# Kernel optimization log

Measured on AMD Instinct MI355X. Metric: run time of the kernel, lower is better.

Reference implementation:

```python
import jax, jax.numpy as jnp
import numpy as np

SHAPES = ((100, 100), (50, 50), (25, 25), (13, 13))
LENS = [h * w for h, w in SHAPES]
STARTS = [0]
for n in LENS[:-1]:
    STARTS.append(STARTS[-1] + n)
S_TOT = sum(LENS)  # 13294
B, C, HH, DH, L, P, NQ, NL, FF = 2, 256, 8, 32, 4, 4, 300, 6, 1024
WH = np.array([[w, h] for h, w in SHAPES], np.float32)  # [L,2] (W,H) offset normalizer


def ln(x, g, b):
    m = x.mean(-1, keepdims=True)
    v = ((x - m) ** 2).mean(-1, keepdims=True)
    return (x - m) * jax.lax.rsqrt(v + 1e-5) * g + b


def bilinear(v, grid):
    # v: [N,Hl,Wl,D]; grid: [N,Q,2] in [-1,1]; grid_sample bilinear, align_corners=False, zero padding
    N, Hl, Wl, Dd = v.shape
    x = (grid[..., 0] + 1.0) * 0.5 * Wl - 0.5
    y = (grid[..., 1] + 1.0) * 0.5 * Hl - 0.5
    x0f = jnp.floor(x); y0f = jnp.floor(y)
    wx = x - x0f; wy = y - y0f
    x0 = x0f.astype(jnp.int32); y0 = y0f.astype(jnp.int32)
    vf = v.reshape(N, Hl * Wl, Dd)
    def g(yi, xi):
        valid = (yi >= 0) & (yi < Hl) & (xi >= 0) & (xi < Wl)
        idx = jnp.clip(yi, 0, Hl - 1) * Wl + jnp.clip(xi, 0, Wl - 1)
        return jnp.take_along_axis(vf, idx[..., None], axis=1) * valid[..., None]
    return (((1 - wy) * (1 - wx))[..., None] * g(y0, x0)
            + ((1 - wy) * wx)[..., None] * g(y0, x0 + 1)
            + (wy * (1 - wx))[..., None] * g(y0 + 1, x0)
            + (wy * wx)[..., None] * g(y0 + 1, x0 + 1))


def msda(query, ref, src, so_w, so_b, aw_w, aw_b, vp_w, vp_b, op_w, op_b):
    # query:[B,Lq,C] ref:[B,Lq,L,2] src:[B,S,C]
    Bq, Lq, _ = query.shape
    value = (src @ vp_w.T + vp_b).reshape(Bq, S_TOT, HH, DH)
    offs = (query @ so_w.T + so_b).reshape(Bq, Lq, HH, L, P, 2)
    aw = jax.nn.softmax((query @ aw_w.T + aw_b).reshape(Bq, Lq, HH, L * P), -1)
    aw = aw.reshape(Bq, Lq, HH, L, P)
    loc = ref[:, :, None, :, None, :] + offs / jnp.asarray(WH)[None, None, None, :, None, :]
    grid = 2.0 * loc - 1.0  # [B,Lq,HH,L,P,2]
    out = jnp.zeros((Bq, HH, Lq, DH), query.dtype)
    for l, (Hl, Wl) in enumerate(SHAPES):
        st = STARTS[l]
        v_l = value[:, st:st + Hl * Wl].reshape(Bq, Hl, Wl, HH, DH).transpose(0, 3, 1, 2, 4).reshape(Bq * HH, Hl, Wl, DH)
        g_l = grid[:, :, :, l].transpose(0, 2, 1, 3, 4).reshape(Bq * HH, Lq * P, 2)
        s = bilinear(v_l, g_l).reshape(Bq, HH, Lq, P, DH)
        out = out + jnp.einsum('bqhp,bhqpd->bhqd', aw[:, :, :, l], s)
    out = out.transpose(0, 2, 1, 3).reshape(Bq, Lq, C)
    return out @ op_w.T + op_b


def enc_ref_points():
    refs = []
    for Hl, Wl in SHAPES:
        ry = (jnp.arange(Hl, dtype=jnp.float32) + 0.5) / Hl
        rx = (jnp.arange(Wl, dtype=jnp.float32) + 0.5) / Wl
        gy, gx = jnp.meshgrid(ry, rx, indexing='ij')
        refs.append(jnp.stack([gx.reshape(-1), gy.reshape(-1)], -1))
    r = jnp.concatenate(refs, 0)  # [S,2]; valid_ratios == 1 (no padding)
    return jnp.broadcast_to(r[None, :, None, :], (B, S_TOT, L, 2))


def _forward(src_flatten, pos_flatten, query_embed, level_embed, refp_w, refp_b,
             eso_w, eso_b, eaw_w, eaw_b, evp_w, evp_b, eop_w, eop_b,
             en1_g, en1_b, el1_w, el1_b, el2_w, el2_b, en2_g, en2_b,
             dso_w, dso_b, daw_w, daw_b, dvp_w, dvp_b, dop_w, dop_b,
             dsa_in_w, dsa_in_b, dsa_out_w, dsa_out_b,
             dn1_g, dn1_b, dn2_g, dn2_b, dn3_g, dn3_b,
             dl1_w, dl1_b, dl2_w, dl2_b):
    lev = jnp.concatenate([jnp.broadcast_to(level_embed[l], (LENS[l], C)) for l in range(L)], 0)
    pos = pos_flatten + lev[None]
    memory = src_flatten
    eref = enc_ref_points()
    for i in range(NL):  # encoder
        q = memory + pos
        m2 = msda(q, eref, memory, eso_w[i], eso_b[i], eaw_w[i], eaw_b[i], evp_w[i], evp_b[i], eop_w[i], eop_b[i])
        memory = ln(memory + m2, en1_g[i], en1_b[i])
        f = jax.nn.relu(memory @ el1_w[i].T + el1_b[i]) @ el2_w[i].T + el2_b[i]
        memory = ln(memory + f, en2_g[i], en2_b[i])
    qpos, tgt = jnp.split(query_embed, 2, axis=-1)
    qpos = jnp.broadcast_to(qpos[None], (B, NQ, C))
    tgt = jnp.broadcast_to(tgt[None], (B, NQ, C))
    ref = jax.nn.sigmoid(qpos @ refp_w.T + refp_b)  # [B,NQ,2]
    init_ref = ref
    ref_in = jnp.broadcast_to(ref[:, :, None, :], (B, NQ, L, 2))
    scale = 1.0 / np.sqrt(DH)
    for i in range(NL):  # decoder
        q = tgt + qpos
        wq, wk, wv = jnp.split(dsa_in_w[i], 3, 0)
        bq, bk, bv = jnp.split(dsa_in_b[i], 3, 0)
        qh = (q @ wq.T + bq).reshape(B, NQ, HH, DH).transpose(0, 2, 1, 3)
        kh = (q @ wk.T + bk).reshape(B, NQ, HH, DH).transpose(0, 2, 1, 3)
        vh = (tgt @ wv.T + bv).reshape(B, NQ, HH, DH).transpose(0, 2, 1, 3)
        att = jax.nn.softmax(jnp.einsum('bhqd,bhkd->bhqk', qh, kh) * scale, -1)
        sa = jnp.einsum('bhqk,bhkd->bhqd', att, vh).transpose(0, 2, 1, 3).reshape(B, NQ, C)
        sa = sa @ dsa_out_w[i].T + dsa_out_b[i]
        tgt = ln(tgt + sa, dn2_g[i], dn2_b[i])
        ca = msda(tgt + qpos, ref_in, memory, dso_w[i], dso_b[i], daw_w[i], daw_b[i], dvp_w[i], dvp_b[i], dop_w[i], dop_b[i])
        tgt = ln(tgt + ca, dn1_g[i], dn1_b[i])
        f = jax.nn.relu(tgt @ dl1_w[i].T + dl1_b[i]) @ dl2_w[i].T + dl2_b[i]
        tgt = ln(tgt + f, dn3_g[i], dn3_b[i])
    return tgt, init_ref, ref


def setup_inputs() -> dict:
    ks = iter(jax.random.split(jax.random.key(0), 80))
    def rn(shape, s=0.02):
        return jax.random.normal(next(ks), shape, jnp.float32) * s
    z = lambda shape: jnp.zeros(shape, jnp.float32)
    o = lambda shape: jnp.ones(shape, jnp.float32)
    HLP2, HLP = HH * L * P * 2, HH * L * P
    return {
        'src_flatten': rn((B, S_TOT, C), 1.0),
        'pos_flatten': rn((B, S_TOT, C), 1.0),
        'query_embed': rn((NQ, 2 * C), 1.0),
        'level_embed': rn((L, C), 1.0),
        'refp_w': rn((2, C)), 'refp_b': z((2,)),
        'eso_w': rn((NL, HLP2, C)), 'eso_b': z((NL, HLP2)),
        'eaw_w': rn((NL, HLP, C)), 'eaw_b': z((NL, HLP)),
        'evp_w': rn((NL, C, C)), 'evp_b': z((NL, C)),
        'eop_w': rn((NL, C, C)), 'eop_b': z((NL, C)),
        'en1_g': o((NL, C)), 'en1_b': z((NL, C)),
        'el1_w': rn((NL, FF, C)), 'el1_b': z((NL, FF)),
        'el2_w': rn((NL, C, FF)), 'el2_b': z((NL, C)),
        'en2_g': o((NL, C)), 'en2_b': z((NL, C)),
        'dso_w': rn((NL, HLP2, C)), 'dso_b': z((NL, HLP2)),
        'daw_w': rn((NL, HLP, C)), 'daw_b': z((NL, HLP)),
        'dvp_w': rn((NL, C, C)), 'dvp_b': z((NL, C)),
        'dop_w': rn((NL, C, C)), 'dop_b': z((NL, C)),
        'dsa_in_w': rn((NL, 3 * C, C)), 'dsa_in_b': z((NL, 3 * C)),
        'dsa_out_w': rn((NL, C, C)), 'dsa_out_b': z((NL, C)),
        'dn1_g': o((NL, C)), 'dn1_b': z((NL, C)),
        'dn2_g': o((NL, C)), 'dn2_b': z((NL, C)),
        'dn3_g': o((NL, C)), 'dn3_b': z((NL, C)),
        'dl1_w': rn((NL, FF, C)), 'dl1_b': z((NL, FF)),
        'dl2_w': rn((NL, C, FF)), 'dl2_b': z((NL, C)),
    }


def reference(src_flatten, pos_flatten, query_embed, level_embed, refp_w, refp_b,
              eso_w, eso_b, eaw_w, eaw_b, evp_w, evp_b, eop_w, eop_b,
              en1_g, en1_b, el1_w, el1_b, el2_w, el2_b, en2_g, en2_b,
              dso_w, dso_b, daw_w, daw_b, dvp_w, dvp_b, dop_w, dop_b,
              dsa_in_w, dsa_in_b, dsa_out_w, dsa_out_b,
              dn1_g, dn1_b, dn2_g, dn2_b, dn3_g, dn3_b,
              dl1_w, dl1_b, dl2_w, dl2_b):
    return _forward(src_flatten, pos_flatten, query_embed, level_embed, refp_w, refp_b,
                    eso_w, eso_b, eaw_w, eaw_b, evp_w, evp_b, eop_w, eop_b,
                    en1_g, en1_b, el1_w, el1_b, el2_w, el2_b, en2_g, en2_b,
                    dso_w, dso_b, daw_w, daw_b, dvp_w, dvp_b, dop_w, dop_b,
                    dsa_in_w, dsa_in_b, dsa_out_w, dsa_out_b,
                    dn1_g, dn1_b, dn2_g, dn2_b, dn3_g, dn3_b,
                    dl1_w, dl1_b, dl2_w, dl2_b)
```

## Files before the change

### kernel.cpp

```cpp
#include <hip/hip_runtime.h>

static constexpr int kS  = 13294;
static constexpr int kB  = 2;
static constexpr int kBS = kB * kS;
static constexpr int kC  = 256;
static constexpr int kH  = 8;
static constexpr int kNQ = 300;
static constexpr int kFF = 1024;
static constexpr int kNL = 6;

using short8 = __attribute__((ext_vector_type(8))) short;
using f32x4  = __attribute__((ext_vector_type(4))) float;

__device__ __forceinline__ unsigned short f2b(float f) {
  unsigned u = __builtin_bit_cast(unsigned, f);
  return (unsigned short)((u + 0x7FFF + ((u >> 16) & 1)) >> 16);
}
__device__ __forceinline__ float bf2f(unsigned short u) {
  return __builtin_bit_cast(float, ((unsigned)u) << 16);
}
__device__ __forceinline__ float bflo(unsigned u) {
  return __builtin_bit_cast(float, u << 16);
}
__device__ __forceinline__ float bfhi(unsigned u) {
  return __builtin_bit_cast(float, u & 0xFFFF0000u);
}

#if defined(__has_builtin)
#if __has_builtin(__builtin_amdgcn_global_load_lds)
#define HAS_GLL 1
#endif
#endif
#ifndef HAS_GLL
#define HAS_GLL 0
#endif

#if HAS_GLL
typedef const __attribute__((address_space(1))) void* gas_t;
typedef __attribute__((address_space(3))) void* las_t;
#define GLOAD16(gp, lp) __builtin_amdgcn_global_load_lds((gas_t)(gp), (las_t)(lp), 16, 0, 0)
#endif

template<int ACT, int OBF>
__global__ __launch_bounds__(256) void gemm_mfma(
    const unsigned short* __restrict__ A, const unsigned short* __restrict__ Wt,
    const float* __restrict__ bias, void* __restrict__ outp, int M, int N, int K) {
  __shared__ __align__(16) unsigned short As[128 * 64];
  __shared__ __align__(16) unsigned short Bs[128 * 64];
  const int t = threadIdx.x;
  const int nB = N >> 7;
  const int tot = gridDim.x;
  const int q8 = tot >> 3, r8 = tot & 7;
  const int xcd = blockIdx.x & 7, pos = blockIdx.x >> 3;
  const int wg = (xcd < r8 ? xcd * (q8 + 1) : r8 * (q8 + 1) + (xcd - r8) * q8) + pos;
  const int m0 = (wg / nB) * 128, n0 = (wg % nB) * 128;
  const int wid = t >> 6, lane = t & 63;
  const int wr = wid >> 1, wc = wid & 1;
  const int srow = t >> 3;
  const int scol = (t & 7) * 8;
  const int lr = lane & 15;
  const int lk = (lane >> 4) * 8;

  f32x4 acc[4][4];
#pragma unroll
  for (int i = 0; i < 4; ++i)
#pragma unroll
    for (int j = 0; j < 4; ++j) acc[i][j] = (f32x4){0.f, 0.f, 0.f, 0.f};

  for (int k0 = 0; k0 < K; k0 += 64) {
#if HAS_GLL
    __syncthreads();
#pragma unroll
    for (int c = 0; c < 4; ++c) {
      int ar = m0 + c * 32 + srow; if (ar >= M) ar = M - 1;
      GLOAD16(A + (size_t)ar * K + k0 + scol, (char*)As + c * 4096 + t * 16);
      int br = n0 + c * 32 + srow; if (br >= N) br = N - 1;
      GLOAD16(Wt + (size_t)br * K + k0 + scol, (char*)Bs + c * 4096 + t * 16);
    }
    __syncthreads();
#else
    short8 ta[4], tb[4];
#pragma unroll
    for (int c = 0; c < 4; ++c) {
      int ar = m0 + c * 32 + srow; if (ar >= M) ar = M - 1;
      ta[c] = *(const short8*)(A + (size_t)ar * K + k0 + scol);
      int br = n0 + c * 32 + srow; if (br >= N) br = N - 1;
      tb[c] = *(const short8*)(Wt + (size_t)br * K + k0 + scol);
    }
    __syncthreads();
#pragma unroll
    for (int c = 0; c < 4; ++c) {
      *(short8*)&As[c * 2048 + t * 8] = ta[c];
      *(short8*)&Bs[c * 2048 + t * 8] = tb[c];
    }
    __syncthreads();
#endif
#pragma unroll
    for (int kk = 0; kk < 2; ++kk) {
      short8 af[4], bf[4];
#pragma unroll
      for (int mi = 0; mi < 4; ++mi)
        af[mi] = *(const short8*)&As[(wr * 64 + mi * 16 + lr) * 64 + kk * 32 + lk];
#pragma unroll
      for (int ni = 0; ni < 4; ++ni)
        bf[ni] = *(const short8*)&Bs[(wc * 64 + ni * 16 + lr) * 64 + kk * 32 + lk];
#pragma unroll
      for (int mi = 0; mi < 4; ++mi)
#pragma unroll
        for (int ni = 0; ni < 4; ++ni)
          acc[mi][ni] = __builtin_amdgcn_mfma_f32_16x16x32_bf16(af[mi], bf[ni], acc[mi][ni], 0, 0, 0);
    }
  }
  const int orow0 = m0 + wr * 64;
  const int ocol = n0 + wc * 64 + (lane & 15);
  float bv[4];
#pragma unroll
  for (int ni = 0; ni < 4; ++ni) bv[ni] = bias[ocol + ni * 16];
#pragma unroll
  for (int mi = 0; mi < 4; ++mi) {
#pragma unroll
    for (int j = 0; j < 4; ++j) {
      const int r = orow0 + mi * 16 + (lane >> 4) * 4 + j;
      if (r < M) {
#pragma unroll
        for (int ni = 0; ni < 4; ++ni) {
          float v = acc[mi][ni][j] + bv[ni];
          if (ACT) v = fmaxf(v, 0.f);
          if (OBF) ((unsigned short*)outp)[(size_t)r * N + ocol + ni * 16] = f2b(v);
          else     ((float*)outp)[(size_t)r * N + ocol + ni * 16] = v;
        }
      }
    }
  }
}

template<int ACT, int OBF>
__global__ __launch_bounds__(256) void gemm_mfma_s(
    const unsigned short* __restrict__ A, const unsigned short* __restrict__ Wt,
    const float* __restrict__ bias, void* __restrict__ outp, int M, int N, int K) {
  __shared__ __align__(16) unsigned short As[64 * 64];
  __shared__ __align__(16) unsigned short Bs[64 * 64];
  const int t = threadIdx.x;
  const int m0 = blockIdx.y * 64, n0 = blockIdx.x * 64;
  const int wid = t >> 6, lane = t & 63;
  const int wr = wid >> 1, wc = wid & 1;
  const int srow = t >> 3;
  const int scol = (t & 7) * 8;
  const int lr = lane & 15;
  const int lk = (lane >> 4) * 8;

  f32x4 acc[2][2];
#pragma unroll
  for (int i = 0; i < 2; ++i)
#pragma unroll
    for (int j = 0; j < 2; ++j) acc[i][j] = (f32x4){0.f, 0.f, 0.f, 0.f};

  for (int k0 = 0; k0 < K; k0 += 64) {
#if HAS_GLL
    __syncthreads();
#pragma unroll
    for (int c = 0; c < 2; ++c) {
      int ar = m0 + c * 32 + srow; if (ar >= M) ar = M - 1;
      GLOAD16(A + (size_t)ar * K + k0 + scol, (char*)As + c * 4096 + t * 16);
      int br = n0 + c * 32 + srow; if (br >= N) br = N - 1;
      GLOAD16(Wt + (size_t)br * K + k0 + scol, (char*)Bs + c * 4096 + t * 16);
    }
    __syncthreads();
#else
    short8 ta[2], tb[2];
#pragma unroll
    for (int c = 0; c < 2; ++c) {
      int ar = m0 + c * 32 + srow; if (ar >= M) ar = M - 1;
      ta[c] = *(const short8*)(A + (size_t)ar * K + k0 + scol);
      int br = n0 + c * 32 + srow; if (br >= N) br = N - 1;
      tb[c] = *(const short8*)(Wt + (size_t)br * K + k0 + scol);
    }
    __syncthreads();
#pragma unroll
    for (int c = 0; c < 2; ++c) {
      *(short8*)&As[c * 2048 + t * 8] = ta[c];
      *(short8*)&Bs[c * 2048 + t * 8] = tb[c];
    }
    __syncthreads();
#endif
#pragma unroll
    for (int kk = 0; kk < 2; ++kk) {
      short8 af[2], bf[2];
#pragma unroll
      for (int mi = 0; mi < 2; ++mi)
        af[mi] = *(const short8*)&As[(wr * 32 + mi * 16 + lr) * 64 + kk * 32 + lk];
#pragma unroll
      for (int ni = 0; ni < 2; ++ni)
        bf[ni] = *(const short8*)&Bs[(wc * 32 + ni * 16 + lr) * 64 + kk * 32 + lk];
#pragma unroll
      for (int mi = 0; mi < 2; ++mi)
#pragma unroll
        for (int ni = 0; ni < 2; ++ni)
          acc[mi][ni] = __builtin_amdgcn_mfma_f32_16x16x32_bf16(af[mi], bf[ni], acc[mi][ni], 0, 0, 0);
    }
  }
  const int orow0 = m0 + wr * 32;
  const int ocol = n0 + wc * 32 + (lane & 15);
  float bv[2];
#pragma unroll
  for (int ni = 0; ni < 2; ++ni) bv[ni] = bias[ocol + ni * 16];
#pragma unroll
  for (int mi = 0; mi < 2; ++mi) {
#pragma unroll
    for (int j = 0; j < 4; ++j) {
      const int r = orow0 + mi * 16 + (lane >> 4) * 4 + j;
      if (r < M) {
#pragma unroll
        for (int ni = 0; ni < 2; ++ni) {
          float v = acc[mi][ni][j] + bv[ni];
          if (ACT) v = fmaxf(v, 0.f);
          if (OBF) ((unsigned short*)outp)[(size_t)r * N + ocol + ni * 16] = f2b(v);
          else     ((float*)outp)[(size_t)r * N + ocol + ni * 16] = v;
        }
      }
    }
  }
}

template<int WRITEQ>
__global__ __launch_bounds__(256) void gemm_ln_k(
    const unsigned short* __restrict__ A, const unsigned short* __restrict__ Wt,
    const float* __restrict__ bias, const float* __restrict__ x,
    const float* __restrict__ g, const float* __restrict__ be,
    float* __restrict__ outf, unsigned short* __restrict__ outb,
    unsigned short* __restrict__ qout, const float* __restrict__ pos,
    const float* __restrict__ lev, int M, int K) {
  __shared__ __align__(16) unsigned short As[64 * 64];
  __shared__ __align__(16) unsigned short Bs[256 * 64];
  __shared__ float rsum[64][4], rsq[64][4], rmv[64][2];
  const int t = threadIdx.x;
  const int m0 = blockIdx.x * 64;
  const int wid = t >> 6, lane = t & 63;
  const int srow = t >> 3;
  const int scol = (t & 7) * 8;
  const int lr = lane & 15;
  const int q4 = lane >> 4;
  const int lk = q4 * 8;

  f32x4 acc[4][4];
#pragma unroll
  for (int i = 0; i < 4; ++i)
#pragma unroll
    for (int j = 0; j < 4; ++j) acc[i][j] = (f32x4){0.f, 0.f, 0.f, 0.f};

  for (int k0 = 0; k0 < K; k0 += 64) {
#if HAS_GLL
    __syncthreads();
#pragma unroll
    for (int c = 0; c < 2; ++c) {
      int ar = m0 + c * 32 + srow; if (ar >= M) ar = M - 1;
      GLOAD16(A + (size_t)ar * K + k0 + scol, (char*)As + c * 4096 + t * 16);
    }
#pragma unroll
    for (int c = 0; c < 8; ++c) {
      GLOAD16(Wt + (size_t)(c * 32 + srow) * K + k0 + scol, (char*)Bs + c * 4096 + t * 16);
    }
    __syncthreads();
#else
    short8 ta[2], tb[8];
#pragma unroll
    for (int c = 0; c < 2; ++c) {
      int ar = m0 + c * 32 + srow; if (ar >= M) ar = M - 1;
      ta[c] = *(const short8*)(A + (size_t)ar * K + k0 + scol);
    }
#pragma unroll
    for (int c = 0; c < 8; ++c)
      tb[c] = *(const short8*)(Wt + (size_t)(c * 32 + srow) * K + k0 + scol);
    __syncthreads();
#pragma unroll
    for (int c = 0; c < 2; ++c) *(short8*)&As[c * 2048 + t * 8] = ta[c];
#pragma unroll
    for (int c = 0; c < 8; ++c) *(short8*)&Bs[c * 2048 + t * 8] = tb[c];
    __syncthreads();
#endif
#pragma unroll
    for (int kk = 0; kk < 2; ++kk) {
      short8 af[4], bf[4];
#pragma unroll
      for (int mi = 0; mi < 4; ++mi)
        af[mi] = *(const short8*)&As[(mi * 16 + lr) * 64 + kk * 32 + lk];
#pragma unroll
      for (int ni = 0; ni < 4; ++ni)
        bf[ni] = *(const short8*)&Bs[(wid * 64 + ni * 16 + lr) * 64 + kk * 32 + lk];
#pragma unroll
      for (int mi = 0; mi < 4; ++mi)
#pragma unroll
        for (int ni = 0; ni < 4; ++ni)
          acc[mi][ni] = __builtin_amdgcn_mfma_f32_16x16x32_bf16(af[mi], bf[ni], acc[mi][ni], 0, 0, 0);
    }
  }
  float bv[4], gv[4], bev[4];
  int cols[4];
#pragma unroll
  for (int ni = 0; ni < 4; ++ni) {
    cols[ni] = wid * 64 + ni * 16 + lr;
    bv[ni] = bias[cols[ni]];
    gv[ni] = g[cols[ni]];
    bev[ni] = be[cols[ni]];
  }
#pragma unroll
  for (int mi = 0; mi < 4; ++mi) {
#pragma unroll
    for (int j = 0; j < 4; ++j) {
      const int brow = mi * 16 + q4 * 4 + j;
      int grow = m0 + brow; if (grow >= M) grow = M - 1;
      const float* xr = x + (size_t)grow * 256;
      float s = 0.f, s2 = 0.f;
#pragma unroll
      for (int ni = 0; ni < 4; ++ni) {
        float v = acc[mi][ni][j] + bv[ni] + xr[cols[ni]];
        acc[mi][ni][j] = v;
        s += v; s2 += v * v;
      }
#pragma unroll
      for (int o = 1; o < 16; o <<= 1) {
        s += __shfl_xor(s, o);
        s2 += __shfl_xor(s2, o);
      }
      if (lr == 0) { rsum[brow][wid] = s; rsq[brow][wid] = s2; }
    }
  }
  __syncthreads();
  if (t < 64) {
    float s = rsum[t][0] + rsum[t][1] + rsum[t][2] + rsum[t][3];
    float s2 = rsq[t][0] + rsq[t][1] + rsq[t][2] + rsq[t][3];
    float mean = s * (1.f / 256.f);
    float var = s2 * (1.f / 256.f) - mean * mean;
    rmv[t][0] = mean;
    rmv[t][1] = rsqrtf(var + 1e-5f);
  }
  __syncthreads();
#pragma unroll
  for (int mi = 0; mi < 4; ++mi) {
#pragma unroll
    for (int j = 0; j < 4; ++j) {
      const int brow = mi * 16 + q4 * 4 + j;
      const int grow = m0 + brow;
      if (grow >= M) continue;
      const float mean = rmv[brow][0], rs = rmv[brow][1];
      int levl = 0;
      if (WRITEQ) {
        int srow_g = (grow >= kS) ? grow - kS : grow;
        levl = (srow_g < 10000) ? 0 : (srow_g < 12500) ? 1 : (srow_g < 13125) ? 2 : 3;
      }
#pragma unroll
      for (int ni = 0; ni < 4; ++ni) {
        const float v = (acc[mi][ni][j] - mean) * rs * gv[ni] + bev[ni];
        const size_t oi = (size_t)grow * 256 + cols[ni];
        outf[oi] = v;
        outb[oi] = f2b(v);
        if (WRITEQ) {
          const float qv = v + pos[oi] + lev[levl * 256 + cols[ni]];
          qout[oi] = f2b(qv);
        }
      }
    }
  }
}

__global__ void cast_bf_k(const float* __restrict__ in, unsigned short* __restrict__ out, int n4) {
  int i = blockIdx.x * 256 + threadIdx.x;
  if (i >= n4) return;
  float4 v = ((const float4*)in)[i];
  ushort4 o; o.x = f2b(v.x); o.y = f2b(v.y); o.z = f2b(v.z); o.w = f2b(v.w);
  ((ushort4*)out)[i] = o;
}

__global__ void copy_cast_k(const float* __restrict__ in, float* __restrict__ outf,
                            unsigned short* __restrict__ outb, int n4) {
  int i = blockIdx.x * 256 + threadIdx.x;
  if (i >= n4) return;
  float4 v = ((const float4*)in)[i];
  ((float4*)outf)[i] = v;
  ushort4 o; o.x = f2b(v.x); o.y = f2b(v.y); o.z = f2b(v.z); o.w = f2b(v.w);
  ((ushort4*)outb)[i] = o;
}

__global__ void pack_bias_k(const float* __restrict__ so_b, const float* __restrict__ aw_b,
                            float* __restrict__ fb) {
  int i = blockIdx.x * 256 + threadIdx.x;
  if (i >= kNL * 384) return;
  int l = i / 384, j = i - l * 384;
  fb[i] = (j < 256) ? so_b[l * 256 + j] : aw_b[l * 128 + j - 256];
}

__global__ void enc_q_k(const float* __restrict__ mem, const float* __restrict__ pos,
                        const float* __restrict__ lev, unsigned short* __restrict__ q, int n4) {
  int i = blockIdx.x * 256 + threadIdx.x;
  if (i >= n4) return;
  int c4 = i & 63;
  int row = i >> 6;
  int s = row % kS;
  int l = (s < 10000) ? 0 : (s < 12500) ? 1 : (s < 13125) ? 2 : 3;
  float4 m = ((const float4*)mem)[i];
  float4 p = ((const float4*)pos)[i];
  float4 lv = ((const float4*)(lev + l * kC))[c4];
  ushort4 o;
  o.x = f2b(m.x + p.x + lv.x); o.y = f2b(m.y + p.y + lv.y);
  o.z = f2b(m.z + p.z + lv.z); o.w = f2b(m.w + p.w + lv.w);
  ((ushort4*)q)[i] = o;
}

__global__ void refs_k(float* __restrict__ refS) {
  int s = blockIdx.x * 256 + threadIdx.x;
  if (s >= kS) return;
  int st, W;
  if (s < 10000)      { st = 0;     W = 100; }
  else if (s < 12500) { st = 10000; W = 50; }
  else if (s < 13125) { st = 12500; W = 25; }
  else                { st = 13125; W = 13; }
  int idx = s - st;
  int y = idx / W;
  int x = idx - y * W;
  refS[s * 2 + 0] = (x + 0.5f) / (float)W;
  refS[s * 2 + 1] = (y + 0.5f) / (float)W;
}

__global__ __launch_bounds__(256) void msda_fused_k(
    const unsigned short* __restrict__ value, int vstride, int vcol,
    const unsigned short* __restrict__ foab, const float* __restrict__ refs,
    unsigned short* __restrict__ out, int Mq) {
  __shared__ int   sidx[16][2][kH][4];
  __shared__ float sw[16][2][kH][4];
  const int t = threadIdx.x;
  const int bq0 = blockIdx.x * 2;
  const int qq = t >> 7;
  {
    const int bq = bq0 + qq;
    const int b = (bq >= Mq) ? 1 : 0;
    const int qi = bq - b * Mq;
    const int h = (t >> 4) & 7, lp = t & 15, l = lp >> 2;
    const unsigned short* row = foab + (size_t)bq * 384;
    float logit = bf2f(row[256 + h * 16 + lp]);
    float mx = logit;
#pragma unroll
    for (int o = 1; o < 16; o <<= 1) mx = fmaxf(mx, __shfl_xor(mx, o));
    float e = __expf(logit - mx), ssum = e;
#pragma unroll
    for (int o = 1; o < 16; o <<= 1) ssum += __shfl_xor(ssum, o);
    const float a = e / ssum;
    const unsigned opair = *(const unsigned*)(row + h * 32 + lp * 2);
    const float offx = bflo(opair);
    const float offy = bfhi(opair);
    const float rx = refs[qi * 2 + 0];
    const float ry = refs[qi * 2 + 1];
    const int wtab[4] = {100, 50, 25, 13};
    const int stab[4] = {0, 10000, 12500, 13125};
    const int W = wtab[l];
    const int start = stab[l];
    const float px = fmaf(rx, (float)W, offx) - 0.5f;
    const float py = fmaf(ry, (float)W, offy) - 0.5f;
    const float fx = floorf(px), fy = floorf(py);
    const float wx = px - fx, wy = py - fy;
    const int x0 = (int)fx, y0 = (int)fy;
    const int x0c = min(max(x0, 0), W - 1);
    const int x1c = min(max(x0 + 1, 0), W - 1);
    const int y0c = min(max(y0, 0), W - 1);
    const int y1c = min(max(y0 + 1, 0), W - 1);
    const float vx0 = (x0 >= 0 && x0 < W) ? 1.f : 0.f;
    const float vx1 = (x0 + 1 >= 0 && x0 + 1 < W) ? 1.f : 0.f;
    const float vy0 = (y0 >= 0 && y0 < W) ? 1.f : 0.f;
    const float vy1 = (y0 + 1 >= 0 && y0 + 1 < W) ? 1.f : 0.f;
    const int base0 = b * kS * vstride + vcol + start * vstride;
    sidx[lp][qq][h][0] = base0 + (y0c * W + x0c) * vstride;
    sidx[lp][qq][h][1] = base0 + (y0c * W + x1c) * vstride;
    sidx[lp][qq][h][2] = base0 + (y1c * W + x0c) * vstride;
    sidx[lp][qq][h][3] = base0 + (y1c * W + x1c) * vstride;
    const float omwx = 1.f - wx, omwy = 1.f - wy;
    sw[lp][qq][h][0] = a * omwy * omwx * vy0 * vx0;
    sw[lp][qq][h][1] = a * omwy * wx * vy0 * vx1;
    sw[lp][qq][h][2] = a * wy * omwx * vy1 * vx0;
    sw[lp][qq][h][3] = a * wy * wx * vy1 * vx1;
  }
  __syncthreads();
  const int h = (t >> 4) & 7, dp = t & 15;
  const int bq = bq0 + qq;
  const int chan = h * 64 + dp * 4;
  const char* valc = (const char*)value;
  float aLo0 = 0.f, aLo1 = 0.f, aHi0 = 0.f, aHi1 = 0.f;
#pragma unroll
  for (int p0 = 0; p0 < 16; p0 += 8) {
    unsigned u[32];
    float w[32];
#pragma unroll
    for (int pp = 0; pp < 8; ++pp) {
      const int4 I = *(const int4*)&sidx[p0 + pp][qq][h][0];
      const float4 Wv = *(const float4*)&sw[p0 + pp][qq][h][0];
      u[pp * 4 + 0] = *(const unsigned*)(valc + (unsigned)(I.x + chan));
      u[pp * 4 + 1] = *(const unsigned*)(valc + (unsigned)(I.y + chan));
      u[pp * 4 + 2] = *(const unsigned*)(valc + (unsigned)(I.z + chan));
      u[pp * 4 + 3] = *(const unsigned*)(valc + (unsigned)(I.w + chan));
      w[pp * 4 + 0] = Wv.x; w[pp * 4 + 1] = Wv.y;
      w[pp * 4 + 2] = Wv.z; w[pp * 4 + 3] = Wv.w;
    }
#pragma unroll
    for (int j = 0; j < 32; j += 2) {
      aLo0 = fmaf(w[j], bflo(u[j]), aLo0);
      aHi0 = fmaf(w[j], bfhi(u[j]), aHi0);
      aLo1 = fmaf(w[j + 1], bflo(u[j + 1]), aLo1);
      aHi1 = fmaf(w[j + 1], bfhi(u[j + 1]), aHi1);
    }
  }
  const float accLo = aLo0 + aLo1;
  const float accHi = aHi0 + aHi1;
  const unsigned packed = (unsigned)f2b(accLo) | ((unsigned)f2b(accHi) << 16);
  ((unsigned*)out)[(size_t)bq * 128 + h * 16 + dp] = packed;
}

__global__ void add_bcast_bf_k(const float* __restrict__ a, const float* __restrict__ b,
                               unsigned short* __restrict__ out, int n4, int nb4) {
  int i = blockIdx.x * 256 + threadIdx.x;
  if (i >= n4) return;
  const float4 av = ((const float4*)a)[i];
  const float4 bv = ((const float4*)b)[i % nb4];
  ushort4 o;
  o.x = f2b(av.x + bv.x); o.y = f2b(av.y + bv.y);
  o.z = f2b(av.z + bv.z); o.w = f2b(av.w + bv.w);
  ((ushort4*)out)[i] = o;
}

__global__ void dec_init_k(const float* __restrict__ qe, float* __restrict__ tgt,
                           unsigned short* __restrict__ tgt_bf, float* __restrict__ qposb) {
  int i = blockIdx.x * 256 + threadIdx.x;
  if (i >= kNQ * kC) return;
  int q = i >> 8, c = i & 255;
  qposb[i] = qe[q * 512 + c];
  float tg = qe[q * 512 + 256 + c];
  tgt[i] = tg;
  tgt[kNQ * kC + i] = tg;
  unsigned short tb = f2b(tg);
  tgt_bf[i] = tb;
  tgt_bf[kNQ * kC + i] = tb;
}

__global__ __launch_bounds__(64) void ref_k(const float* __restrict__ qposb,
                                            const float* __restrict__ rw,
                                            const float* __restrict__ rb,
                                            float* __restrict__ ref300) {
  const int q = blockIdx.x;
  const int lane = threadIdx.x;
  const float4 qv = ((const float4*)(qposb + q * 256))[lane];
  const float4 w0 = ((const float4*)rw)[lane];
  const float4 w1 = ((const float4*)(rw + 256))[lane];
  float a0 = qv.x * w0.x + qv.y * w0.y + qv.z * w0.z + qv.w * w0.w;
  float a1 = qv.x * w1.x + qv.y * w1.y + qv.z * w1.z + qv.w * w1.w;
#pragma unroll
  for (int off = 32; off; off >>= 1) {
    a0 += __shfl_xor(a0, off);
    a1 += __shfl_xor(a1, off);
  }
  if (lane == 0) {
    ref300[q * 2 + 0] = 1.f / (1.f + __expf(-(a0 + rb[0])));
    ref300[q * 2 + 1] = 1.f / (1.f + __expf(-(a1 + rb[1])));
  }
}

__global__ __launch_bounds__(64) void dec_attn_k(const float* __restrict__ qk,
                                                 const float* __restrict__ v,
                                                 unsigned short* __restrict__ outp) {
  const int bid = blockIdx.x;
  const int q = bid % kNQ;
  const int bh = bid / kNQ;
  const int h = bh & 7;
  const int b = bh >> 3;
  const int lane = threadIdx.x;
  __shared__ float p[304];
  const float* qv = qk + ((size_t)(b * kNQ + q)) * 512 + h * 32;
  float qreg[32];
#pragma unroll
  for (int m = 0; m < 32; ++m) qreg[m] = qv[m];
  float scores[5];
  float mx = -1e30f;
#pragma unroll
  for (int j = 0; j < 5; ++j) {
    const int k = lane + j * 64;
    float sc = -1e30f;
    if (k < kNQ) {
      const float* kv = qk + ((size_t)(b * kNQ + k)) * 512 + 256 + h * 32;
      float acc = 0.f;
#pragma unroll
      for (int m = 0; m < 32; ++m) acc = fmaf(qreg[m], kv[m], acc);
      sc = acc * 0.17677669529663687f;
    }
    scores[j] = sc;
    mx = fmaxf(mx, sc);
  }
#pragma unroll
  for (int off = 32; off; off >>= 1) mx = fmaxf(mx, __shfl_xor(mx, off));
  float sum = 0.f;
#pragma unroll
  for (int j = 0; j < 5; ++j) {
    const int k = lane + j * 64;
    float e = 0.f;
    if (k < kNQ) e = __expf(scores[j] - mx);
    scores[j] = e;
    sum += e;
  }
#pragma unroll
  for (int off = 32; off; off >>= 1) sum += __shfl_xor(sum, off);
  const float inv = 1.f / sum;
#pragma unroll
  for (int j = 0; j < 5; ++j) {
    const int k = lane + j * 64;
    if (k < kNQ) p[k] = scores[j] * inv;
  }
  __syncthreads();
  const int d = lane & 31, half = lane >> 5;
  float acc = 0.f;
  for (int k = half * 150; k < half * 150 + 150; ++k)
    acc = fmaf(p[k], v[((size_t)(b * kNQ + k)) * 256 + h * 32 + d], acc);
  acc += __shfl_down(acc, 32);
  if (lane < 32) outp[((size_t)(b * kNQ + q)) * 256 + h * 32 + d] = f2b(acc);
}

__global__ void write_refs_k(const float* __restrict__ ref300, float* __restrict__ outp) {
  int i = blockIdx.x * 256 + threadIdx.x;
  if (i >= 1200) return;
  float v = ref300[i % 600];
  outp[153600 + i] = v;
  outp[154800 + i] = v;
}

__global__ void sentinel_k(float* __restrict__ outp) {
  if (threadIdx.x < 64) outp[threadIdx.x] = 12345.0f;
}

extern "C" void kernel_launch(void* const* d_in, const int* in_sizes, int n_in,
                              void* d_out, int out_size, void* d_ws, size_t ws_size,
                              hipStream_t stream) {
  const float* src      = (const float*)d_in[0];
  const float* pos      = (const float*)d_in[1];
  const float* qe       = (const float*)d_in[2];
  const float* lev      = (const float*)d_in[3];
  const float* refp_w   = (const float*)d_in[4];
  const float* refp_b   = (const float*)d_in[5];
  const float* eso_w    = (const float*)d_in[6];
  const float* eso_b    = (const float*)d_in[7];
  const float* eaw_w    = (const float*)d_in[8];
  const float* eaw_b    = (const float*)d_in[9];
  const float* evp_w    = (const float*)d_in[10];
  const float* evp_b    = (const float*)d_in[11];
  const float* eop_w    = (const float*)d_in[12];
  const float* eop_b    = (const float*)d_in[13];
  const float* en1_g    = (const float*)d_in[14];
  const float* en1_b    = (const float*)d_in[15];
  const float* el1_w    = (const float*)d_in[16];
  const float* el1_b    = (const float*)d_in[17];
  const float* el2_w    = (const float*)d_in[18];
  const float* el2_b    = (const float*)d_in[19];
  const float* en2_g    = (const float*)d_in[20];
  const float* en2_b    = (const float*)d_in[21];
  const float* dso_w    = (const float*)d_in[22];
  const float* dso_b    = (const float*)d_in[23];
  const float* daw_w    = (const float*)d_in[24];
  const float* daw_b    = (const float*)d_in[25];
  const float* dvp_w    = (const float*)d_in[26];
  const float* dvp_b    = (const float*)d_in[27];
  const float* dop_w    = (const float*)d_in[28];
  const float* dop_b    = (const float*)d_in[29];
  const float* dsa_in_w = (const float*)d_in[30];
  const float* dsa_in_b = (const float*)d_in[31];
  const float* dsa_out_w= (const float*)d_in[32];
  const float* dsa_out_b= (const float*)d_in[33];
  const float* dn1_g    = (const float*)d_in[34];
  const float* dn1_b    = (const float*)d_in[35];
  const float* dn2_g    = (const float*)d_in[36];
  const float* dn2_b    = (const float*)d_in[37];
  const float* dn3_g    = (const float*)d_in[38];
  const float* dn3_b    = (const float*)d_in[39];
  const float* dl1_w    = (const float*)d_in[40];
  const float* dl1_b    = (const float*)d_in[41];
  const float* dl2_w    = (const float*)d_in[42];
  const float* dl2_b    = (const float*)d_in[43];

  float* Wsp = (float*)d_ws;
  size_t off = 0;
  auto alloc = [&](size_t n) { float* p = Wsp + off; off += n; return p; };
  const size_t NBC = (size_t)kBS * kC;
  float* memory   = alloc(NBC);
  unsigned short* memory_bf = (unsigned short*)alloc(NBC / 2);
  float* r2       = alloc(NBC);
  unsigned short* val_bf = (unsigned short*)r2;
  float* r3       = alloc(NBC / 2);
  unsigned short* qbuf_bf = (unsigned short*)r3;
  unsigned short* sampbuf_bf = (unsigned short*)r3;
  float* r4       = alloc(NBC * 2);
  unsigned short* foab_bf = (unsigned short*)r4;
  unsigned short* hid_bf = (unsigned short*)r4;
  unsigned short* val_all = (unsigned short*)r2;
  float* refS     = alloc((size_t)kS * 2 + 2);
  auto allocb = [&](size_t elems) { return (unsigned short*)alloc(elems / 2); };
  unsigned short* fesoawW = allocb((size_t)kNL * 384 * 256);
  unsigned short* evpW  = allocb((size_t)kNL * 65536);
  unsigned short* eopW  = allocb((size_t)kNL * 65536);
  unsigned short* el1W  = allocb((size_t)kNL * 262144);
  unsigned short* el2W  = allocb((size_t)kNL * 262144);
  unsigned short* fdsoawW = allocb((size_t)kNL * 384 * 256);
  unsigned short* dvpW  = allocb((size_t)kNL * 65536);
  unsigned short* dopW  = allocb((size_t)kNL * 65536);
  unsigned short* dsaiW = allocb((size_t)kNL * 196608);
  unsigned short* dsaoW = allocb((size_t)kNL * 65536);
  unsigned short* dl1W  = allocb((size_t)kNL * 262144);
  unsigned short* dl2W  = allocb((size_t)kNL * 262144);
  float* fbias_e  = alloc((size_t)kNL * 384);
  float* fbias_d  = alloc((size_t)kNL * 384);
  const size_t NQC = (size_t)kB * kNQ * kC;
  float* tgt      = alloc(NQC);
  unsigned short* tgt_bf = (unsigned short*)alloc(NQC / 2);
  float* qposb    = alloc((size_t)kNQ * kC);
  unsigned short* dq_bf = (unsigned short*)alloc(NQC / 2);
  float* qkbuf    = alloc(NQC * 2);
  float* vbuf     = alloc(NQC);
  unsigned short* sabuf_bf = (unsigned short*)alloc(NQC / 2);
  unsigned short* dfoab_bf = (unsigned short*)alloc((size_t)kB * kNQ * 384 / 2);
  unsigned short* dsamp_bf = (unsigned short*)alloc(NQC / 2);
  unsigned short* dffnh_bf = (unsigned short*)alloc((size_t)kB * kNQ * kFF / 2);
  float* ref300   = alloc(600);

  if (ws_size < off * sizeof(float)) {
    hipLaunchKernelGGL(sentinel_k, dim3(1), dim3(64), 0, stream, (float*)d_out);
    return;
  }

  auto GEMM = [&](const unsigned short* A, const unsigned short* Wt, const float* bias,
                  void* out, int M, int N, int K, int variant) {
    dim3 g((N / 128) * ((M + 127) / 128));
    if (variant == 1)
      hipLaunchKernelGGL((gemm_mfma<1, 1>), g, dim3(256), 0, stream, A, Wt, bias, out, M, N, K);
    else if (variant == 2)
      hipLaunchKernelGGL((gemm_mfma<0, 1>), g, dim3(256), 0, stream, A, Wt, bias, out, M, N, K);
    else
      hipLaunchKernelGGL((gemm_mfma<0, 0>), g, dim3(256), 0, stream, A, Wt, bias, out, M, N, K);
  };
  auto GEMMS = [&](const unsigned short* A, const unsigned short* Wt, const float* bias,
                   void* out, int M, int N, int K, int variant) {
    dim3 g(N / 64, (M + 63) / 64);
    if (variant == 1)
      hipLaunchKernelGGL((gemm_mfma_s<1, 1>), g, dim3(256), 0, stream, A, Wt, bias, out, M, N, K);
    else if (variant == 2)
      hipLaunchKernelGGL((gemm_mfma_s<0, 1>), g, dim3(256), 0, stream, A, Wt, bias, out, M, N, K);
    else
      hipLaunchKernelGGL((gemm_mfma_s<0, 0>), g, dim3(256), 0, stream, A, Wt, bias, out, M, N, K);
  };
  auto CASTW = [&](const float* srcw, unsigned short* dstw, size_t elems) {
    int n4 = (int)(elems / 4);
    hipLaunchKernelGGL(cast_bf_k, dim3((n4 + 255) / 256), dim3(256), 0, stream, srcw, dstw, n4);
  };

  for (int i = 0; i < kNL; ++i) {
    CASTW(eso_w + (size_t)i * 65536, fesoawW + (size_t)i * 98304, 65536);
    CASTW(eaw_w + (size_t)i * 32768, fesoawW + (size_t)i * 98304 + 65536, 32768);
    CASTW(dso_w + (size_t)i * 65536, fdsoawW + (size_t)i * 98304, 65536);
    CASTW(daw_w + (size_t)i * 32768, fdsoawW + (size_t)i * 98304 + 65536, 32768);
  }
  CASTW(evp_w, evpW, (size_t)kNL * 65536);
  CASTW(eop_w, eopW, (size_t)kNL * 65536);
  CASTW(el1_w, el1W, (size_t)kNL * 262144);
  CASTW(el2_w, el2W, (size_t)kNL * 262144);
  CASTW(dvp_w, dvpW, (size_t)kNL * 65536);
  CASTW(dop_w, dopW, (size_t)kNL * 65536);
  CASTW(dsa_in_w, dsaiW, (size_t)kNL * 196608);
  CASTW(dsa_out_w, dsaoW, (size_t)kNL * 65536);
  CASTW(dl1_w, dl1W, (size_t)kNL * 262144);
  CASTW(dl2_w, dl2W, (size_t)kNL * 262144);
  hipLaunchKernelGGL(pack_bias_k, dim3((kNL * 384 + 255) / 256), dim3(256), 0, stream,
                     eso_b, eaw_b, fbias_e);
  hipLaunchKernelGGL(pack_bias_k, dim3((kNL * 384 + 255) / 256), dim3(256), 0, stream,
                     dso_b, daw_b, fbias_d);
  const int n4full = kBS * 64;
  hipLaunchKernelGGL(copy_cast_k, dim3((n4full + 255) / 256), dim3(256), 0, stream,
                     src, memory, memory_bf, n4full);
  hipLaunchKernelGGL(refs_k, dim3((kS + 255) / 256), dim3(256), 0, stream, refS);
  hipLaunchKernelGGL(enc_q_k, dim3((n4full + 255) / 256), dim3(256), 0, stream,
                     memory, pos, lev, qbuf_bf, n4full);

  const int grid_ln = (kBS + 63) / 64;
  for (int i = 0; i < kNL; ++i) {
    GEMM(memory_bf, evpW + (size_t)i * 65536, evp_b + i * kC, val_bf, kBS, 256, 256, 2);
    GEMM(qbuf_bf, fesoawW + (size_t)i * 98304, fbias_e + i * 384, foab_bf, kBS, 384, 256, 2);
    hipLaunchKernelGGL(msda_fused_k, dim3(kBS / 2), dim3(256), 0, stream,
                       val_bf, 512, 0, foab_bf, refS, sampbuf_bf, kS);
    hipLaunchKernelGGL((gemm_ln_k<0>), dim3(grid_ln), dim3(256), 0, stream,
                       sampbuf_bf, eopW + (size_t)i * 65536, eop_b + i * kC,
                       memory, en1_g + i * kC, en1_b + i * kC,
                       memory, memory_bf, (unsigned short*)nullptr,
                       (const float*)nullptr, (const float*)nullptr, kBS, 256);
    GEMM(memory_bf, el1W + (size_t)i * 262144, el1_b + i * kFF, hid_bf, kBS, 1024, 256, 1);
    hipLaunchKernelGGL((gemm_ln_k<1>), dim3(grid_ln), dim3(256), 0, stream,
                       hid_bf, el2W + (size_t)i * 262144, el2_b + i * kC,
                       memory, en2_g + i * kC, en2_b + i * kC,
                       memory, memory_bf, qbuf_bf, pos, lev, kBS, 1024);
  }

  hipLaunchKernelGGL(dec_init_k, dim3(300), dim3(256), 0, stream, qe, tgt, tgt_bf, qposb);
  hipLaunchKernelGGL(ref_k, dim3(kNQ), dim3(64), 0, stream, qposb, refp_w, refp_b, ref300);
  GEMM(memory_bf, dvpW, dvp_b, val_all, kBS, kNL * 256, 256, 2);

  const int dn4 = kB * kNQ * 64;
  const int qn4 = kNQ * 64;
  const int MD = kB * kNQ;
  const int grid_lnd = (MD + 63) / 64;
  for (int i = 0; i < kNL; ++i) {
    hipLaunchKernelGGL(add_bcast_bf_k, dim3((dn4 + 255) / 256), dim3(256), 0, stream,
                       tgt, qposb, dq_bf, dn4, qn4);
    GEMMS(dq_bf, dsaiW + (size_t)i * 196608, dsa_in_b + i * 768, qkbuf, MD, 512, 256, 0);
    GEMMS(tgt_bf, dsaiW + (size_t)i * 196608 + (size_t)512 * 256,
          dsa_in_b + i * 768 + 512, vbuf, MD, 256, 256, 0);
    hipLaunchKernelGGL(dec_attn_k, dim3(kB * kH * kNQ), dim3(64), 0, stream,
                       qkbuf, vbuf, sabuf_bf);
    hipLaunchKernelGGL((gemm_ln_k<0>), dim3(grid_lnd), dim3(256), 0, stream,
                       sabuf_bf, dsaoW + (size_t)i * 65536, dsa_out_b + i * kC,
                       tgt, dn2_g + i * kC, dn2_b + i * kC,
                       tgt, tgt_bf, (unsigned short*)nullptr,
                       (const float*)nullptr, (const float*)nullptr, MD, 256);
    hipLaunchKernelGGL(add_bcast_bf_k, dim3((dn4 + 255) / 256), dim3(256), 0, stream,
                       tgt, qposb, dq_bf, dn4, qn4);
    GEMMS(dq_bf, fdsoawW + (size_t)i * 98304, fbias_d + i * 384, dfoab_bf, MD, 384, 256, 2);
    hipLaunchKernelGGL(msda_fused_k, dim3(MD / 2), dim3(256), 0, stream,
                       val_all, kNL * 512, i * 512, dfoab_bf, ref300, dsamp_bf, kNQ);
    hipLaunchKernelGGL((gemm_ln_k<0>), dim3(grid_lnd), dim3(256), 0, stream,
                       dsamp_bf, dopW + (size_t)i * 65536, dop_b + i * kC,
                       tgt, dn1_g + i * kC, dn1_b + i * kC,
                       tgt, tgt_bf, (unsigned short*)nullptr,
                       (const float*)nullptr, (const float*)nullptr, MD, 256);
    GEMMS(tgt_bf, dl1W + (size_t)i * 262144, dl1_b + i * kFF, dffnh_bf, MD, 1024, 256, 1);
    hipLaunchKernelGGL((gemm_ln_k<0>), dim3(grid_lnd), dim3(256), 0, stream,
                       dffnh_bf, dl2W + (size_t)i * 262144, dl2_b + i * kC,
                       tgt, dn3_g + i * kC, dn3_b + i * kC,
                       tgt, tgt_bf, (unsigned short*)nullptr,
                       (const float*)nullptr, (const float*)nullptr, MD, 1024);
  }

  hipMemcpyAsync(d_out, tgt, NQC * sizeof(float), hipMemcpyDeviceToDevice, stream);
  hipLaunchKernelGGL(write_refs_k, dim3(5), dim3(256), 0, stream, ref300, (float*)d_out);
}
```

Measured before the change: 2.051 ms.

## Keep encoder residual stream in bf16 only and halve GEMM-LN row tile

Drops the fp32 encoder memory buffer: the fused GEMM+LayerNorm now reads the residual input as bf16 and writes only bf16 output unless WRITEF is set. Precomputes pos+level embedding once as a bf16 buffer instead of recomputing level index and reading two fp32 arrays every layer. Also shrinks the GEMM-LN tile from 64 to 32 rows so more blocks launch. This cuts memory traffic per encoder layer but loses precision in the residual stream, since the residual is rounded to bf16 every layer, and the decoder's residual input is also read from bf16.

```diff
diff --git a/kernel.cpp b/kernel.cpp
--- a/kernel.cpp
+++ b/kernel.cpp
@@ -222,19 +222,19 @@
   }
 }
 
-template<int WRITEQ>
+template<int WRITEQ, int WRITEF>
 __global__ __launch_bounds__(256) void gemm_ln_k(
     const unsigned short* __restrict__ A, const unsigned short* __restrict__ Wt,
-    const float* __restrict__ bias, const float* __restrict__ x,
+    const float* __restrict__ bias, const unsigned short* __restrict__ x_bf,
     const float* __restrict__ g, const float* __restrict__ be,
     float* __restrict__ outf, unsigned short* __restrict__ outb,
-    unsigned short* __restrict__ qout, const float* __restrict__ pos,
-    const float* __restrict__ lev, int M, int K) {
-  __shared__ __align__(16) unsigned short As[64 * 64];
+    unsigned short* __restrict__ qout, const unsigned short* __restrict__ poslev,
+    int M, int K) {
+  __shared__ __align__(16) unsigned short As[32 * 64];
   __shared__ __align__(16) unsigned short Bs[256 * 64];
-  __shared__ float rsum[64][4], rsq[64][4], rmv[64][2];
+  __shared__ float rsum[32][4], rsq[32][4], rmv[32][2];
   const int t = threadIdx.x;
-  const int m0 = blockIdx.x * 64;
+  const int m0 = blockIdx.x * 32;
   const int wid = t >> 6, lane = t & 63;
   const int srow = t >> 3;
   const int scol = (t & 7) * 8;
@@ -242,19 +242,18 @@
   const int q4 = lane >> 4;
   const int lk = q4 * 8;
 
-  f32x4 acc[4][4];
-#pragma unroll
-  for (int i = 0; i < 4; ++i)
+  f32x4 acc[2][4];
+#pragma unroll
+  for (int i = 0; i < 2; ++i)
 #pragma unroll
     for (int j = 0; j < 4; ++j) acc[i][j] = (f32x4){0.f, 0.f, 0.f, 0.f};
 
   for (int k0 = 0; k0 < K; k0 += 64) {
 #if HAS_GLL
     __syncthreads();
-#pragma unroll
-    for (int c = 0; c < 2; ++c) {
-      int ar = m0 + c * 32 + srow; if (ar >= M) ar = M - 1;
-      GLOAD16(A + (size_t)ar * K + k0 + scol, (char*)As + c * 4096 + t * 16);
+    {
+      int ar = m0 + srow; if (ar >= M) ar = M - 1;
+      GLOAD16(A + (size_t)ar * K + k0 + scol, (char*)As + t * 16);
     }
 #pragma unroll
     for (int c = 0; c < 8; ++c) {
@@ -262,33 +261,31 @@
     }
     __syncthreads();
 #else
-    short8 ta[2], tb[8];
-#pragma unroll
-    for (int c = 0; c < 2; ++c) {
-      int ar = m0 + c * 32 + srow; if (ar >= M) ar = M - 1;
-      ta[c] = *(const short8*)(A + (size_t)ar * K + k0 + scol);
+    short8 ta, tb[8];
+    {
+      int ar = m0 + srow; if (ar >= M) ar = M - 1;
+      ta = *(const short8*)(A + (size_t)ar * K + k0 + scol);
     }
 #pragma unroll
     for (int c = 0; c < 8; ++c)
       tb[c] = *(const short8*)(Wt + (size_t)(c * 32 + srow) * K + k0 + scol);
     __syncthreads();
-#pragma unroll
-    for (int c = 0; c < 2; ++c) *(short8*)&As[c * 2048 + t * 8] = ta[c];
+    *(short8*)&As[t * 8] = ta;
 #pragma unroll
     for (int c = 0; c < 8; ++c) *(short8*)&Bs[c * 2048 + t * 8] = tb[c];
     __syncthreads();
 #endif
 #pragma unroll
     for (int kk = 0; kk < 2; ++kk) {
-      short8 af[4], bf[4];
-#pragma unroll
-      for (int mi = 0; mi < 4; ++mi)
+      short8 af[2], bf[4];
+#pragma unroll
+      for (int mi = 0; mi < 2; ++mi)
         af[mi] = *(const short8*)&As[(mi * 16 + lr) * 64 + kk * 32 + lk];
 #pragma unroll
       for (int ni = 0; ni < 4; ++ni)
         bf[ni] = *(const short8*)&Bs[(wid * 64 + ni * 16 + lr) * 64 + kk * 32 + lk];
 #pragma unroll
-      for (int mi = 0; mi < 4; ++mi)
+      for (int mi = 0; mi < 2; ++mi)
 #pragma unroll
         for (int ni = 0; ni < 4; ++ni)
           acc[mi][ni] = __builtin_amdgcn_mfma_f32_16x16x32_bf16(af[mi], bf[ni], acc[mi][ni], 0, 0, 0);
@@ -304,16 +301,16 @@
     bev[ni] = be[cols[ni]];
   }
 #pragma unroll
-  for (int mi = 0; mi < 4; ++mi) {
+  for (int mi = 0; mi < 2; ++mi) {
 #pragma unroll
     for (int j = 0; j < 4; ++j) {
       const int brow = mi * 16 + q4 * 4 + j;
       int grow = m0 + brow; if (grow >= M) grow = M - 1;
-      const float* xr = x + (size_t)grow * 256;
+      const unsigned short* xr = x_bf + (size_t)grow * 256;
       float s = 0.f, s2 = 0.f;
 #pragma unroll
       for (int ni = 0; ni < 4; ++ni) {
-        float v = acc[mi][ni][j] + bv[ni] + xr[cols[ni]];
+        float v = acc[mi][ni][j] + bv[ni] + bf2f(xr[cols[ni]]);
         acc[mi][ni][j] = v;
         s += v; s2 += v * v;
       }
@@ -326,7 +323,7 @@
     }
   }
   __syncthreads();
-  if (t < 64) {
+  if (t < 32) {
     float s = rsum[t][0] + rsum[t][1] + rsum[t][2] + rsum[t][3];
     float s2 = rsq[t][0] + rsq[t][1] + rsq[t][2] + rsq[t][3];
     float mean = s * (1.f / 256.f);
@@ -336,28 +333,20 @@
   }
   __syncthreads();
 #pragma unroll
-  for (int mi = 0; mi < 4; ++mi) {
+  for (int mi = 0; mi < 2; ++mi) {
 #pragma unroll
     for (int j = 0; j < 4; ++j) {
       const int brow = mi * 16 + q4 * 4 + j;
       const int grow = m0 + brow;
       if (grow >= M) continue;
       const float mean = rmv[brow][0], rs = rmv[brow][1];
-      int levl = 0;
-      if (WRITEQ) {
-        int srow_g = (grow >= kS) ? grow - kS : grow;
-        levl = (srow_g < 10000) ? 0 : (srow_g < 12500) ? 1 : (srow_g < 13125) ? 2 : 3;
-      }
 #pragma unroll
       for (int ni = 0; ni < 4; ++ni) {
         const float v = (acc[mi][ni][j] - mean) * rs * gv[ni] + bev[ni];
         const size_t oi = (size_t)grow * 256 + cols[ni];
-        outf[oi] = v;
+        if (WRITEF) outf[oi] = v;
         outb[oi] = f2b(v);
-        if (WRITEQ) {
-          const float qv = v + pos[oi] + lev[levl * 256 + cols[ni]];
-          qout[oi] = f2b(qv);
-        }
+        if (WRITEQ) qout[oi] = f2b(v + bf2f(poslev[oi]));
       }
     }
   }
@@ -371,16 +360,6 @@
   ((ushort4*)out)[i] = o;
 }
 
-__global__ void copy_cast_k(const float* __restrict__ in, float* __restrict__ outf,
-                            unsigned short* __restrict__ outb, int n4) {
-  int i = blockIdx.x * 256 + threadIdx.x;
-  if (i >= n4) return;
-  float4 v = ((const float4*)in)[i];
-  ((float4*)outf)[i] = v;
-  ushort4 o; o.x = f2b(v.x); o.y = f2b(v.y); o.z = f2b(v.z); o.w = f2b(v.w);
-  ((ushort4*)outb)[i] = o;
-}
-
 __global__ void pack_bias_k(const float* __restrict__ so_b, const float* __restrict__ aw_b,
                             float* __restrict__ fb) {
   int i = blockIdx.x * 256 + threadIdx.x;
@@ -389,20 +368,31 @@
   fb[i] = (j < 256) ? so_b[l * 256 + j] : aw_b[l * 128 + j - 256];
 }
 
-__global__ void enc_q_k(const float* __restrict__ mem, const float* __restrict__ pos,
-                        const float* __restrict__ lev, unsigned short* __restrict__ q, int n4) {
+__global__ void poslev_k(const float* __restrict__ pos, const float* __restrict__ lev,
+                         unsigned short* __restrict__ out, int n4) {
   int i = blockIdx.x * 256 + threadIdx.x;
   if (i >= n4) return;
   int c4 = i & 63;
   int row = i >> 6;
   int s = row % kS;
   int l = (s < 10000) ? 0 : (s < 12500) ? 1 : (s < 13125) ? 2 : 3;
-  float4 m = ((const float4*)mem)[i];
   float4 p = ((const float4*)pos)[i];
   float4 lv = ((const float4*)(lev + l * kC))[c4];
   ushort4 o;
-  o.x = f2b(m.x + p.x + lv.x); o.y = f2b(m.y + p.y + lv.y);
-  o.z = f2b(m.z + p.z + lv.z); o.w = f2b(m.w + p.w + lv.w);
+  o.x = f2b(p.x + lv.x); o.y = f2b(p.y + lv.y);
+  o.z = f2b(p.z + lv.z); o.w = f2b(p.w + lv.w);
+  ((ushort4*)out)[i] = o;
+}
+
+__global__ void enc_q_k(const float* __restrict__ src, const unsigned short* __restrict__ poslev,
+                        unsigned short* __restrict__ q, int n4) {
+  int i = blockIdx.x * 256 + threadIdx.x;
+  if (i >= n4) return;
+  float4 m = ((const float4*)src)[i];
+  ushort4 pl = ((const ushort4*)poslev)[i];
+  ushort4 o;
+  o.x = f2b(m.x + bf2f(pl.x)); o.y = f2b(m.y + bf2f(pl.y));
+  o.z = f2b(m.z + bf2f(pl.z)); o.w = f2b(m.w + bf2f(pl.w));
   ((ushort4*)q)[i] = o;
 }
 
@@ -682,8 +672,8 @@
   size_t off = 0;
   auto alloc = [&](size_t n) { float* p = Wsp + off; off += n; return p; };
   const size_t NBC = (size_t)kBS * kC;
-  float* memory   = alloc(NBC);
   unsigned short* memory_bf = (unsigned short*)alloc(NBC / 2);
+  unsigned short* poslev_bf = (unsigned short*)alloc(NBC / 2);
   float* r2       = alloc(NBC);
   unsigned short* val_bf = (unsigned short*)r2;
   float* r3       = alloc(NBC / 2);
@@ -773,28 +763,30 @@
   hipLaunchKernelGGL(pack_bias_k, dim3((kNL * 384 + 255) / 256), dim3(256), 0, stream,
                      dso_b, daw_b, fbias_d);
   const int n4full = kBS * 64;
-  hipLaunchKernelGGL(copy_cast_k, dim3((n4full + 255) / 256), dim3(256), 0, stream,
-                     src, memory, memory_bf, n4full);
+  hipLaunchKernelGGL(cast_bf_k, dim3((n4full + 255) / 256), dim3(256), 0, stream,
+                     src, memory_bf, n4full);
+  hipLaunchKernelGGL(poslev_k, dim3((n4full + 255) / 256), dim3(256), 0, stream,
+                     pos, lev, poslev_bf, n4full);
   hipLaunchKernelGGL(refs_k, dim3((kS + 255) / 256), dim3(256), 0, stream, refS);
   hipLaunchKernelGGL(enc_q_k, dim3((n4full + 255) / 256), dim3(256), 0, stream,
-                     memory, pos, lev, qbuf_bf, n4full);
-
-  const int grid_ln = (kBS + 63) / 64;
+                     src, poslev_bf, qbuf_bf, n4full);
+
+  const int grid_ln = (kBS + 31) / 32;
   for (int i = 0; i < kNL; ++i) {
     GEMM(memory_bf, evpW + (size_t)i * 65536, evp_b + i * kC, val_bf, kBS, 256, 256, 2);
     GEMM(qbuf_bf, fesoawW + (size_t)i * 98304, fbias_e + i * 384, foab_bf, kBS, 384, 256, 2);
     hipLaunchKernelGGL(msda_fused_k, dim3(kBS / 2), dim3(256), 0, stream,
                        val_bf, 512, 0, foab_bf, refS, sampbuf_bf, kS);
-    hipLaunchKernelGGL((gemm_ln_k<0>), dim3(grid_ln), dim3(256), 0, stream,
+    hipLaunchKernelGGL((gemm_ln_k<0, 0>), dim3(grid_ln), dim3(256), 0, stream,
                        sampbuf_bf, eopW + (size_t)i * 65536, eop_b + i * kC,
-                       memory, en1_g + i * kC, en1_b + i * kC,
-                       memory, memory_bf, (unsigned short*)nullptr,
-                       (const float*)nullptr, (const float*)nullptr, kBS, 256);
+                       memory_bf, en1_g + i * kC, en1_b + i * kC,
+                       (float*)nullptr, memory_bf, (unsigned short*)nullptr,
+                       (const unsigned short*)nullptr, kBS, 256);
     GEMM(memory_bf, el1W + (size_t)i * 262144, el1_b + i * kFF, hid_bf, kBS, 1024, 256, 1);
-    hipLaunchKernelGGL((gemm_ln_k<1>), dim3(grid_ln), dim3(256), 0, stream,
+    hipLaunchKernelGGL((gemm_ln_k<1, 0>), dim3(grid_ln), dim3(256), 0, stream,
                        hid_bf, el2W + (size_t)i * 262144, el2_b + i * kC,
-                       memory, en2_g + i * kC, en2_b + i * kC,
-                       memory, memory_bf, qbuf_bf, pos, lev, kBS, 1024);
+                       memory_bf, en2_g + i * kC, en2_b + i * kC,
+                       (float*)nullptr, memory_bf, qbuf_bf, poslev_bf, kBS, 1024);
   }
 
   hipLaunchKernelGGL(dec_init_k, dim3(300), dim3(256), 0, stream, qe, tgt, tgt_bf, qposb);
@@ -804,7 +796,7 @@
   const int dn4 = kB * kNQ * 64;
   const int qn4 = kNQ * 64;
   const int MD = kB * kNQ;
-  const int grid_lnd = (MD + 63) / 64;
+  const int grid_lnd = (MD + 31) / 32;
   for (int i = 0; i < kNL; ++i) {
     hipLaunchKernelGGL(add_bcast_bf_k, dim3((dn4 + 255) / 256), dim3(256), 0, stream,
                        tgt, qposb, dq_bf, dn4, qn4);
@@ -813,27 +805,27 @@
           dsa_in_b + i * 768 + 512, vbuf, MD, 256, 256, 0);
     hipLaunchKernelGGL(dec_attn_k, dim3(kB * kH * kNQ), dim3(64), 0, stream,
                        qkbuf, vbuf, sabuf_bf);
-    hipLaunchKernelGGL((gemm_ln_k<0>), dim3(grid_lnd), dim3(256), 0, stream,
+    hipLaunchKernelGGL((gemm_ln_k<0, 1>), dim3(grid_lnd), dim3(256), 0, stream,
                        sabuf_bf, dsaoW + (size_t)i * 65536, dsa_out_b + i * kC,
-                       tgt, dn2_g + i * kC, dn2_b + i * kC,
+                       tgt_bf, dn2_g + i * kC, dn2_b + i * kC,
                        tgt, tgt_bf, (unsigned short*)nullptr,
-                       (const float*)nullptr, (const float*)nullptr, MD, 256);
+                       (const unsigned short*)nullptr, MD, 256);
     hipLaunchKernelGGL(add_bcast_bf_k, dim3((dn4 + 255) / 256), dim3(256), 0, stream,
                        tgt, qposb, dq_bf, dn4, qn4);
     GEMMS(dq_bf, fdsoawW + (size_t)i * 98304, fbias_d + i * 384, dfoab_bf, MD, 384, 256, 2);
     hipLaunchKernelGGL(msda_fused_k, dim3(MD / 2), dim3(256), 0, stream,
                        val_all, kNL * 512, i * 512, dfoab_bf, ref300, dsamp_bf, kNQ);
-    hipLaunchKernelGGL((gemm_ln_k<0>), dim3(grid_lnd), dim3(256), 0, stream,
+    hipLaunchKernelGGL((gemm_ln_k<0, 1>), dim3(grid_lnd), dim3(256), 0, stream,
                        dsamp_bf, dopW + (size_t)i * 65536, dop_b + i * kC,
-                       tgt, dn1_g + i * kC, dn1_b + i * kC,
+                       tgt_bf, dn1_g + i * kC, dn1_b + i * kC,
                        tgt, tgt_bf, (unsigned short*)nullptr,
-                       (const float*)nullptr, (const float*)nullptr, MD, 256);
+                       (const unsigned short*)nullptr, MD, 256);
     GEMMS(tgt_bf, dl1W + (size_t)i * 262144, dl1_b + i * kFF, dffnh_bf, MD, 1024, 256, 1);
-    hipLaunchKernelGGL((gemm_ln_k<0>), dim3(grid_lnd), dim3(256), 0, stream,
+    hipLaunchKernelGGL((gemm_ln_k<0, 1>), dim3(grid_lnd), dim3(256), 0, stream,
                        dffnh_bf, dl2W + (size_t)i * 262144, dl2_b + i * kC,
-                       tgt, dn3_g + i * kC, dn3_b + i * kC,
+                       tgt_bf, dn3_g + i * kC, dn3_b + i * kC,
                        tgt, tgt_bf, (unsigned short*)nullptr,
-                       (const float*)nullptr, (const float*)nullptr, MD, 1024);
+                       (const unsigned short*)nullptr, MD, 1024);
   }
 
   hipMemcpyAsync(d_out, tgt, NQC * sizeof(float), hipMemcpyDeviceToDevice, stream);
```

New measurement: 1.953 ms. -4.8%, faster.
